# Kernel tuning notes

Hardware: AMD Instinct MI355X
Metric: run time of the kernel (lower is better)

Reference implementation:

```python
import jax, jax.numpy as jnp
import numpy as np

N = 1048576          # total nodes across batched graphs
NUM_SEGMENTS = 2048  # number of graphs in the batch
D = 128              # node_net hidden width

leaky = jax.nn.leaky_relu  # slope 0.01, matches torch nn.LeakyReLU default


def _seg_mean(x, seg_ids):
    # dgl.mean_nodes: per-graph mean over ragged node segments
    sums = jax.ops.segment_sum(x, seg_ids, num_segments=NUM_SEGMENTS)
    cnt = jax.ops.segment_sum(jnp.ones((x.shape[0], 1), x.dtype), seg_ids,
                              num_segments=NUM_SEGMENTS)
    return sums / jnp.maximum(cnt, 1.0)  # guard empty graphs


def setup_inputs() -> dict:
    key = jax.random.key(0)
    ks = jax.random.split(key, 20)
    feat = jax.random.normal(ks[0], (N, 3), dtype=jnp.float32)
    segment_ids = jnp.sort(jax.random.randint(ks[1], (N,), 0, NUM_SEGMENTS)).astype(jnp.int32)
    s = 0.05
    p = {
        'feat': feat, 'segment_ids': segment_ids,
        # net1: 3 -> D -> D (LeakyReLU after each, incl. final activation)
        'W1a': jax.random.normal(ks[2], (3, D)) * s,  'b1a': jnp.zeros((D,)),
        'W1b': jax.random.normal(ks[3], (D, D)) * s,  'b1b': jnp.zeros((D,)),
        # net2..net5: single Linear D->D + LeakyReLU
        'W2': jax.random.normal(ks[4], (D, D)) * s,   'b2': jnp.zeros((D,)),
        'W3': jax.random.normal(ks[5], (D, D)) * s,   'b3': jnp.zeros((D,)),
        'W4': jax.random.normal(ks[6], (D, D)) * s,   'b4': jnp.zeros((D,)),
        'W5': jax.random.normal(ks[7], (D, D)) * s,   'b5': jnp.zeros((D,)),
        # outputnet: D -> 64 (LeakyReLU) -> 1 (no final activation)
        'Wo1': jax.random.normal(ks[8], (D, 64)) * s, 'bo1': jnp.zeros((64,)),
        'Wo2': jax.random.normal(ks[9], (64, 1)) * s, 'bo2': jnp.zeros((1,)),
    }
    return p


def reference(feat, segment_ids, W1a, b1a, W1b, b1b, W2, b2, W3, b3,
              W4, b4, W5, b5, Wo1, bo1, Wo2, bo2):
    seg = segment_ids
    # net1: Linear+LeakyReLU, Linear, final LeakyReLU
    h = leaky(leaky(feat @ W1a + b1a) @ W1b + b1b)
    h = h + _seg_mean(h, seg)[seg]            # mean_nodes + broadcast + residual
    h = leaky(h @ W2 + b2)                    # net2
    h = h + _seg_mean(h, seg)[seg]
    h = leaky(h @ W3 + b3)                    # net3
    h = h + _seg_mean(h, seg)[seg]
    h = leaky(h @ W4 + b4)                    # net4
    h = h + _seg_mean(h, seg)[seg]
    h = leaky(h @ W5 + b5)                    # net5
    g = _seg_mean(h, seg)                     # final per-graph mean [G, D]
    energy = leaky(g @ Wo1 + bo1) @ Wo2 + bo2 # outputnet, no final activation
    return energy.squeeze(-1)                 # [G]
```

## Files before the change

kernel.cpp:

```cpp
#include <hip/hip_runtime.h>
#include <stdint.h>

#define NSEG 2048
#define NTOT 1048576
#define CAP  624
#define BLK  512
#define H_BYTES (CAP * 256)
#define CS_OFF    H_BYTES
#define LBIAS_OFF (H_BYTES + 1024)
#define WBUF_OFF  (H_BYTES + 1024 + 512)
#define LDS_BYTES (H_BYTES + 1024 + 512 + 2048)

typedef __bf16 bf16x8 __attribute__((ext_vector_type(8)));
typedef __bf16 bf16x4 __attribute__((ext_vector_type(4)));
typedef float  f32x4  __attribute__((ext_vector_type(4)));

__device__ __forceinline__ float leaky(float v) { return fmaxf(v, 0.01f * v); }
__device__ __forceinline__ uint32_t haddr(int row, int bytecol) {
    return ((uint32_t)row * 256u + (uint32_t)bytecol) ^ (((uint32_t)row & 7u) << 4);
}

__global__ void seg_offsets_kernel(const int* __restrict__ seg, int* __restrict__ offs) {
    int t = blockIdx.x * blockDim.x + threadIdx.x;
    if (t > NSEG) return;
    int lo = 0, hi = NTOT;
    while (lo < hi) { int mid = (lo + hi) >> 1; if (seg[mid] < t) lo = mid + 1; else hi = mid; }
    offs[t] = lo;
}

__global__ void wconv_kernel(const float* __restrict__ W1b, const float* __restrict__ W2,
                             const float* __restrict__ W3,  const float* __restrict__ W4,
                             const float* __restrict__ W5,  __bf16* __restrict__ wt) {
    int idx = blockIdx.x * blockDim.x + threadIdx.x;
    int m = idx >> 14, e = idx & 16383;
    int nn = e >> 7, kk = e & 127;
    const float* W = (m == 0) ? W1b : (m == 1) ? W2 : (m == 2) ? W3 : (m == 3) ? W4 : W5;
    wt[idx] = (__bf16)W[kk * 128 + nn];
}

extern __shared__ char smem[];

__global__ __launch_bounds__(BLK, 2) __attribute__((amdgpu_waves_per_eu(2, 2)))
void fused_pflow(
    const float* __restrict__ feat, const int* __restrict__ offs,
    const __bf16* __restrict__ wt5,
    const float* __restrict__ W1a, const float* __restrict__ b1a,
    const float* __restrict__ Wl0, const float* __restrict__ bl0,
    const float* __restrict__ Wl1, const float* __restrict__ bl1,
    const float* __restrict__ Wl2, const float* __restrict__ bl2,
    const float* __restrict__ Wl3, const float* __restrict__ bl3,
    const float* __restrict__ Wl4, const float* __restrict__ bl4,
    const float* __restrict__ Wo1, const float* __restrict__ bo1,
    const float* __restrict__ Wo2, const float* __restrict__ bo2,
    float* __restrict__ out)
{
    const int s    = blockIdx.x;
    const int tid  = threadIdx.x;
    const int lane = tid & 63;
    const int wave = tid >> 6;
    const int lm   = lane & 15;
    const int lq   = lane >> 4;

    char*  sm    = smem;
    float* cs0   = (float*)(sm + CS_OFF);
    float* cs1   = cs0 + 128;
    float* lbias = (float*)(sm + LBIAS_OFF);
    float* wbuf  = (float*)(sm + WBUF_OFF);

    const int g0 = offs[s];
    int n = offs[s + 1] - g0;
    n = n < CAP ? n : CAP;

    for (int i = tid; i < 512; i += BLK) {
        int ch = i >> 2, j = i & 3;
        wbuf[i] = (j < 3) ? W1a[j * 128 + ch] : b1a[ch];
    }
    if (tid < 256) cs0[tid] = 0.f;
    __syncthreads();

    for (int i = tid; i < n; i += BLK) {
        float f0 = feat[(g0 + i) * 3 + 0];
        float f1 = feat[(g0 + i) * 3 + 1];
        float f2 = feat[(g0 + i) * 3 + 2];
        #pragma unroll
        for (int c0 = 0; c0 < 128; c0 += 8) {
            bf16x8 pk;
            #pragma unroll
            for (int j = 0; j < 8; ++j) {
                const f32x4 w = *(const f32x4*)&wbuf[(c0 + j) * 4];
                pk[j] = (__bf16)leaky(fmaf(f0, w[0], fmaf(f1, w[1], fmaf(f2, w[2], w[3]))));
            }
            *(bf16x8*)(sm + haddr(i, c0 * 2)) = pk;
        }
    }

    const int   ntiles = (n + 15) >> 4;
    const float inv_n  = 1.f / (float)(n > 1 ? n : 1);

    for (int L = 0; L < 5; ++L) {
        __syncthreads();
        float* csCur  = (L & 1) ? cs1 : cs0;
        float* csPrev = (L & 1) ? cs0 : cs1;
        if (L == 0) {
            if (tid < 128) lbias[tid] = bl0[tid];
        } else {
            const float* Wc = (L == 1) ? Wl1 : (L == 2) ? Wl2 : (L == 3) ? Wl3 : Wl4;
            const float* bc = (L == 1) ? bl1 : (L == 2) ? bl2 : (L == 3) ? bl3 : bl4;
            const int ch = tid >> 2, q = tid & 3;
            float sacc = 0.f;
            #pragma unroll 8
            for (int i = 0; i < 32; ++i) {
                const int k = q * 32 + i;
                sacc = fmaf(csPrev[k], Wc[k * 128 + ch], sacc);
            }
            sacc += __shfl_xor(sacc, 1);
            sacc += __shfl_xor(sacc, 2);
            if (q == 0) lbias[ch] = fmaf(inv_n, sacc, bc[ch]);
            if (tid < 128) csCur[tid] = 0.f;
        }
        __syncthreads();

        const __bf16* wt = wt5 + L * 16384;
        bf16x8 afrag[8][4];
        #pragma unroll
        for (int ct = 0; ct < 8; ++ct)
            #pragma unroll
            for (int ks = 0; ks < 4; ++ks)
                afrag[ct][ks] = *(const bf16x8*)(wt + (ct * 16 + lm) * 128 + ks * 32 + lq * 8);
        f32x4 lbreg[8];
        #pragma unroll
        for (int ct = 0; ct < 8; ++ct)
            lbreg[ct] = *(const f32x4*)&lbias[ct * 16 + lq * 4];

        float creg[8][4] = {};
        for (int rt = wave; rt < ntiles; rt += 8) {
            const int node = rt * 16 + lm;
            bf16x8 bfrag[4];
            #pragma unroll
            for (int ks = 0; ks < 4; ++ks)
                bfrag[ks] = *(const bf16x8*)(sm + haddr(node, ks * 64 + lq * 16));
            f32x4 acc[8];
            #pragma unroll
            for (int ct = 0; ct < 8; ++ct) acc[ct] = lbreg[ct];
            #pragma unroll
            for (int ks = 0; ks < 4; ++ks)
                #pragma unroll
                for (int ct = 0; ct < 8; ++ct)
                    acc[ct] = __builtin_amdgcn_mfma_f32_16x16x32_bf16(afrag[ct][ks], bfrag[ks], acc[ct], 0, 0, 0);
            if (node < n) {
                #pragma unroll
                for (int ct = 0; ct < 8; ++ct) {
                    bf16x4 pk;
                    #pragma unroll
                    for (int i = 0; i < 4; ++i) {
                        float v = leaky(acc[ct][i]);
                        creg[ct][i] += v;
                        pk[i] = (__bf16)v;
                    }
                    *(bf16x4*)(sm + haddr(node, (ct * 16 + lq * 4) * 2)) = pk;
                }
            }
        }
        #pragma unroll
        for (int ct = 0; ct < 8; ++ct)
            #pragma unroll
            for (int i = 0; i < 4; ++i) {
                float v = creg[ct][i];
                v += __shfl_xor(v, 1); v += __shfl_xor(v, 2);
                v += __shfl_xor(v, 4); v += __shfl_xor(v, 8);
                if (lm == 0) atomicAdd(&csCur[ct * 16 + lq * 4 + i], v);
            }
    }
    __syncthreads();

    if (wave == 0) {
        float a = bo1[lane];
        for (int k = 0; k < 128; ++k)
            a = fmaf(cs0[k] * inv_n, Wo1[k * 64 + lane], a);
        a = leaky(a);
        float e = a * Wo2[lane];
        e += __shfl_xor(e, 32); e += __shfl_xor(e, 16); e += __shfl_xor(e, 8);
        e += __shfl_xor(e, 4);  e += __shfl_xor(e, 2);  e += __shfl_xor(e, 1);
        if (lane == 0) out[s] = e + bo2[0];
    }
}

extern "C" void kernel_launch(void* const* d_in, const int* in_sizes, int n_in,
                              void* d_out, int out_size, void* d_ws, size_t ws_size,
                              hipStream_t stream) {
    (void)in_sizes; (void)n_in; (void)out_size; (void)ws_size;
    const float* feat = (const float*)d_in[0];
    const int*   seg  = (const int*)d_in[1];
    const float* W1a  = (const float*)d_in[2];
    const float* b1a  = (const float*)d_in[3];
    const float* W1b  = (const float*)d_in[4];
    const float* b1b  = (const float*)d_in[5];
    const float* W2   = (const float*)d_in[6];
    const float* b2   = (const float*)d_in[7];
    const float* W3   = (const float*)d_in[8];
    const float* b3   = (const float*)d_in[9];
    const float* W4   = (const float*)d_in[10];
    const float* b4   = (const float*)d_in[11];
    const float* W5   = (const float*)d_in[12];
    const float* b5   = (const float*)d_in[13];
    const float* Wo1  = (const float*)d_in[14];
    const float* bo1  = (const float*)d_in[15];
    const float* Wo2  = (const float*)d_in[16];
    const float* bo2  = (const float*)d_in[17];
    float* out = (float*)d_out;

    __bf16* wt = (__bf16*)d_ws;
    int* offs = (int*)((char*)d_ws + 5 * 16384 * sizeof(__bf16));

    seg_offsets_kernel<<<(NSEG + 256) / 256, 256, 0, stream>>>(seg, offs);
    wconv_kernel<<<(5 * 16384) / 256, 256, 0, stream>>>(W1b, W2, W3, W4, W5, wt);

    hipFuncSetAttribute((const void*)fused_pflow,
                        hipFuncAttributeMaxDynamicSharedMemorySize, LDS_BYTES);
    fused_pflow<<<NSEG, BLK, LDS_BYTES, stream>>>(feat, offs, wt, W1a, b1a,
                                                  W1b, b1b, W2, b2, W3, b3,
                                                  W4, b4, W5, b5,
                                                  Wo1, bo1, Wo2, bo2, out);
}
```

Before: 855.2 us.

## Split GEMM work across 16 waves by row and column groups

Doubles the block to 1024 threads and splits the 16 waves into 4 column groups times 4 row groups, so each wave computes only 2 of the 8 output column tiles. Because columns are now split, layer outputs are held in registers, followed by a block barrier, and only then written back to LDS in place. The aim is more resident waves for latency hiding and lower register pressure, since A fragments shrink from 32 to 8 vectors. In exchange, each wave re-reads the full input rows from LDS (four times the LDS read traffic overall) and adds an extra barrier per layer. Column sums are now taken from bf16-rounded values, and the bias-from-mean step is reworked for 8 lanes per channel.

```diff
diff --git a/kernel.cpp b/kernel.cpp
--- a/kernel.cpp
+++ b/kernel.cpp
@@ -4,7 +4,8 @@
 #define NSEG 2048
 #define NTOT 1048576
 #define CAP  624
-#define BLK  512
+#define BLK  1024
+#define MAX_RT 10
 #define H_BYTES (CAP * 256)
 #define CS_OFF    H_BYTES
 #define LBIAS_OFF (H_BYTES + 1024)
@@ -40,7 +41,7 @@
 
 extern __shared__ char smem[];
 
-__global__ __launch_bounds__(BLK, 2) __attribute__((amdgpu_waves_per_eu(2, 2)))
+__global__ __launch_bounds__(BLK, 4)
 void fused_pflow(
     const float* __restrict__ feat, const int* __restrict__ offs,
     const __bf16* __restrict__ wt5,
@@ -60,6 +61,8 @@
     const int wave = tid >> 6;
     const int lm   = lane & 15;
     const int lq   = lane >> 4;
+    const int cg   = wave & 3;
+    const int rg   = wave >> 2;
 
     char*  sm    = smem;
     float* cs0   = (float*)(sm + CS_OFF);
@@ -71,19 +74,21 @@
     int n = offs[s + 1] - g0;
     n = n < CAP ? n : CAP;
 
-    for (int i = tid; i < 512; i += BLK) {
-        int ch = i >> 2, j = i & 3;
-        wbuf[i] = (j < 3) ? W1a[j * 128 + ch] : b1a[ch];
+    if (tid < 512) {
+        int ch = tid >> 2, j = tid & 3;
+        wbuf[tid] = (j < 3) ? W1a[j * 128 + ch] : b1a[ch];
     }
     if (tid < 256) cs0[tid] = 0.f;
     __syncthreads();
 
-    for (int i = tid; i < n; i += BLK) {
+    for (int idx = tid; idx < n * 2; idx += BLK) {
+        const int i = idx >> 1, half = idx & 1;
         float f0 = feat[(g0 + i) * 3 + 0];
         float f1 = feat[(g0 + i) * 3 + 1];
         float f2 = feat[(g0 + i) * 3 + 2];
         #pragma unroll
-        for (int c0 = 0; c0 < 128; c0 += 8) {
+        for (int cc = 0; cc < 8; ++cc) {
+            const int c0 = half * 64 + cc * 8;
             bf16x8 pk;
             #pragma unroll
             for (int j = 0; j < 8; ++j) {
@@ -96,6 +101,8 @@
 
     const int   ntiles = (n + 15) >> 4;
     const float inv_n  = 1.f / (float)(n > 1 ? n : 1);
+    const int   ct0    = cg * 2;
+    const int   cnt    = (ntiles > rg) ? ((ntiles - rg + 3) >> 2) : 0;
 
     for (int L = 0; L < 5; ++L) {
         __syncthreads();
@@ -106,70 +113,89 @@
         } else {
             const float* Wc = (L == 1) ? Wl1 : (L == 2) ? Wl2 : (L == 3) ? Wl3 : Wl4;
             const float* bc = (L == 1) ? bl1 : (L == 2) ? bl2 : (L == 3) ? bl3 : bl4;
-            const int ch = tid >> 2, q = tid & 3;
+            const int ch = tid >> 3, q = tid & 7;
             float sacc = 0.f;
-            #pragma unroll 8
-            for (int i = 0; i < 32; ++i) {
-                const int k = q * 32 + i;
+            #pragma unroll
+            for (int i = 0; i < 16; ++i) {
+                const int k = q * 16 + i;
                 sacc = fmaf(csPrev[k], Wc[k * 128 + ch], sacc);
             }
             sacc += __shfl_xor(sacc, 1);
             sacc += __shfl_xor(sacc, 2);
+            sacc += __shfl_xor(sacc, 4);
             if (q == 0) lbias[ch] = fmaf(inv_n, sacc, bc[ch]);
             if (tid < 128) csCur[tid] = 0.f;
         }
         __syncthreads();
 
         const __bf16* wt = wt5 + L * 16384;
-        bf16x8 afrag[8][4];
-        #pragma unroll
-        for (int ct = 0; ct < 8; ++ct)
+        bf16x8 afrag[2][4];
+        #pragma unroll
+        for (int c = 0; c < 2; ++c)
             #pragma unroll
             for (int ks = 0; ks < 4; ++ks)
-                afrag[ct][ks] = *(const bf16x8*)(wt + (ct * 16 + lm) * 128 + ks * 32 + lq * 8);
-        f32x4 lbreg[8];
-        #pragma unroll
-        for (int ct = 0; ct < 8; ++ct)
-            lbreg[ct] = *(const f32x4*)&lbias[ct * 16 + lq * 4];
-
-        float creg[8][4] = {};
-        for (int rt = wave; rt < ntiles; rt += 8) {
-            const int node = rt * 16 + lm;
-            bf16x8 bfrag[4];
-            #pragma unroll
-            for (int ks = 0; ks < 4; ++ks)
-                bfrag[ks] = *(const bf16x8*)(sm + haddr(node, ks * 64 + lq * 16));
-            f32x4 acc[8];
-            #pragma unroll
-            for (int ct = 0; ct < 8; ++ct) acc[ct] = lbreg[ct];
-            #pragma unroll
-            for (int ks = 0; ks < 4; ++ks)
+                afrag[c][ks] = *(const bf16x8*)(wt + ((ct0 + c) * 16 + lm) * 128 + ks * 32 + lq * 8);
+        f32x4 lbreg[2];
+        #pragma unroll
+        for (int c = 0; c < 2; ++c)
+            lbreg[c] = *(const f32x4*)&lbias[(ct0 + c) * 16 + lq * 4];
+
+        bf16x4 hreg[MAX_RT][2];
+        #pragma unroll
+        for (int j = 0; j < MAX_RT; ++j) {
+            if (j < cnt) {
+                const int node = (rg + 4 * j) * 16 + lm;
+                bf16x8 bfrag[4];
                 #pragma unroll
-                for (int ct = 0; ct < 8; ++ct)
-                    acc[ct] = __builtin_amdgcn_mfma_f32_16x16x32_bf16(afrag[ct][ks], bfrag[ks], acc[ct], 0, 0, 0);
-            if (node < n) {
+                for (int ks = 0; ks < 4; ++ks)
+                    bfrag[ks] = *(const bf16x8*)(sm + haddr(node, ks * 64 + lq * 16));
+                f32x4 acc0 = lbreg[0], acc1 = lbreg[1];
                 #pragma unroll
-                for (int ct = 0; ct < 8; ++ct) {
-                    bf16x4 pk;
+                for (int ks = 0; ks < 4; ++ks) {
+                    acc0 = __builtin_amdgcn_mfma_f32_16x16x32_bf16(afrag[0][ks], bfrag[ks], acc0, 0, 0, 0);
+                    acc1 = __builtin_amdgcn_mfma_f32_16x16x32_bf16(afrag[1][ks], bfrag[ks], acc1, 0, 0, 0);
+                }
+                bf16x4 p0, p1;
+                #pragma unroll
+                for (int i = 0; i < 4; ++i) {
+                    p0[i] = (__bf16)leaky(acc0[i]);
+                    p1[i] = (__bf16)leaky(acc1[i]);
+                }
+                hreg[j][0] = p0;
+                hreg[j][1] = p1;
+            }
+            __builtin_amdgcn_sched_barrier(0);
+        }
+        __syncthreads();
+
+        float csum0[4] = {}, csum1[4] = {};
+        #pragma unroll
+        for (int j = 0; j < MAX_RT; ++j) {
+            if (j < cnt) {
+                const int node = (rg + 4 * j) * 16 + lm;
+                if (node < n) {
+                    *(bf16x4*)(sm + haddr(node, (ct0 * 16 + lq * 4) * 2))       = hreg[j][0];
+                    *(bf16x4*)(sm + haddr(node, ((ct0 + 1) * 16 + lq * 4) * 2)) = hreg[j][1];
                     #pragma unroll
                     for (int i = 0; i < 4; ++i) {
-                        float v = leaky(acc[ct][i]);
-                        creg[ct][i] += v;
-                        pk[i] = (__bf16)v;
+                        csum0[i] += (float)hreg[j][0][i];
+                        csum1[i] += (float)hreg[j][1][i];
                     }
-                    *(bf16x4*)(sm + haddr(node, (ct * 16 + lq * 4) * 2)) = pk;
                 }
             }
         }
         #pragma unroll
-        for (int ct = 0; ct < 8; ++ct)
-            #pragma unroll
-            for (int i = 0; i < 4; ++i) {
-                float v = creg[ct][i];
-                v += __shfl_xor(v, 1); v += __shfl_xor(v, 2);
-                v += __shfl_xor(v, 4); v += __shfl_xor(v, 8);
-                if (lm == 0) atomicAdd(&csCur[ct * 16 + lq * 4 + i], v);
-            }
+        for (int i = 0; i < 4; ++i) {
+            float v0 = csum0[i], v1 = csum1[i];
+            v0 += __shfl_xor(v0, 1); v0 += __shfl_xor(v0, 2);
+            v0 += __shfl_xor(v0, 4); v0 += __shfl_xor(v0, 8);
+            v1 += __shfl_xor(v1, 1); v1 += __shfl_xor(v1, 2);
+            v1 += __shfl_xor(v1, 4); v1 += __shfl_xor(v1, 8);
+            if (lm == 0) {
+                atomicAdd(&csCur[ct0 * 16 + lq * 4 + i], v0);
+                atomicAdd(&csCur[(ct0 + 1) * 16 + lq * 4 + i], v1);
+            }
+        }
     }
     __syncthreads();
 
```

New measurement: 1.184 ms. 1.38x slower.
